# Kernel optimization log

Measured on AMD Instinct MI355X. Metric: run time of the kernel, lower is better.

Reference implementation:

```python
import jax, jax.numpy as jnp
import numpy as np

B, T, C = 8, 4096, 256
N_LAYER, LAYER_ID = 12, 5


def setup_inputs() -> dict:
    key = jax.random.key(0)
    ks = jax.random.split(key, 5)
    x = jax.random.normal(ks[0], (B, T, C), dtype=jnp.float32)
    scale = 1.0 / np.sqrt(C)
    Wk = jax.random.normal(ks[1], (C, C), jnp.float32) * scale
    Wv = jax.random.normal(ks[2], (C, C), jnp.float32) * scale
    Wr = jax.random.normal(ks[3], (C, C), jnp.float32) * scale
    Wo = jax.random.normal(ks[4], (C, C), jnp.float32) * scale
    # 'fancy' init from _init_weights
    ratio_0_to_1 = LAYER_ID / (N_LAYER - 1)
    h = np.arange(C, dtype=np.float64)
    decay = -5.0 + 8.0 * (h / (C - 1)) ** (0.7 + 1.3 * ratio_0_to_1)
    zigzag = ((np.arange(C) + 1) % 3 - 1) * 0.5
    first = np.log(0.3) + zigzag
    return dict(
        x=x, Wk=Wk, Wv=Wv, Wr=Wr, Wo=Wo,
        spatial_decay=jnp.asarray(decay, jnp.float32),
        spatial_first=jnp.asarray(first, jnp.float32),
        ln_w=jnp.ones((C,), jnp.float32),
        ln_b=jnp.zeros((C,), jnp.float32),
    )


def _wkv(w, u, k, v):
    # Numerically-stable RWKV WKV scan, matching wkv_cuda forward.
    # w, u: [C] (already divided by T); k, v: [B, T, C]. Returns y: [B, T, C].
    MIN_VALUE = -1e38

    def step(carry, kv):
        p, q, o = carry            # [B, C] each
        kt, vt = kv                # [B, C]
        no = jnp.maximum(o, u + kt)
        a = jnp.exp(o - no)
        b = jnp.exp(u + kt - no)
        y = (a * p + b * vt) / (a * q + b)
        no2 = jnp.maximum(w + o, kt)
        a2 = jnp.exp(w + o - no2)
        b2 = jnp.exp(kt - no2)
        return (a2 * p + b2 * vt, a2 * q + b2, no2), y

    p0 = jnp.zeros(k.shape[0:1] + k.shape[2:3], k.dtype)  # [B, C]
    q0 = jnp.zeros_like(p0)
    o0 = jnp.full_like(p0, MIN_VALUE)
    kT = jnp.swapaxes(k, 0, 1)  # [T, B, C]
    vT = jnp.swapaxes(v, 0, 1)
    _, yT = jax.lax.scan(step, (p0, q0, o0), (kT, vT))
    return jnp.swapaxes(yT, 0, 1)


def _layernorm(x, w, b, eps=1e-5):
    mu = jnp.mean(x, axis=-1, keepdims=True)
    xc = x - mu
    var = jnp.mean(xc * xc, axis=-1, keepdims=True)
    return xc * jax.lax.rsqrt(var + eps) * w + b


def reference(x, Wk, Wv, Wr, Wo, spatial_decay, spatial_first, ln_w, ln_b):
    # shift_pixel == 0 -> xk = xv = xr = x (module's own code path)
    t = x.shape[1]
    k = jnp.einsum('btc,dc->btd', x, Wk)
    v = jnp.einsum('btc,dc->btd', x, Wv)
    r = jnp.einsum('btc,dc->btd', x, Wr)
    sr = jax.nn.sigmoid(r)
    y = _wkv(spatial_decay / t, spatial_first / t, k, v)
    y = _layernorm(y, ln_w, ln_b)
    return jnp.einsum('btc,dc->btd', sr * y, Wo)
```

## Files before the change

kernel.cpp:

```cpp
#include <hip/hip_runtime.h>
#include <cstdint>
#include <cstddef>

#define B_ 8
#define T_ 4096
#define C_ 256
#define NC_ 256
#define L_ (T_ / NC_)
#define M_ (B_ * T_)

typedef float f32x4 __attribute__((ext_vector_type(4)));
typedef short bf16x8 __attribute__((ext_vector_type(8)));

__device__ __forceinline__ unsigned short f2b(float f) {
    unsigned int u = __float_as_uint(f);
    u += 0x7fffu + ((u >> 16) & 1u);
    return (unsigned short)(u >> 16);
}
__device__ __forceinline__ float b2f(unsigned short h) {
    return __uint_as_float(((unsigned int)h) << 16);
}

__global__ __launch_bounds__(256) void cvt_w(const float* __restrict__ Wk,
                                             const float* __restrict__ Wv,
                                             const float* __restrict__ Wr,
                                             const float* __restrict__ Wo,
                                             unsigned short* __restrict__ wb) {
    const int r = blockIdx.x;
    const int mat = r >> 5;
    const float* src = (mat == 0) ? Wk : (mat == 1) ? Wv : (mat == 2) ? Wr : Wo;
    unsigned short* dst = wb + (size_t)mat * 65536;
    const size_t i = (size_t)(r & 31) * 2048 + (size_t)threadIdx.x * 8;
    float4 a = *(const float4*)(src + i);
    float4 b = *(const float4*)(src + i + 4);
    bf16x8 o;
    o[0] = (short)f2b(a.x); o[1] = (short)f2b(a.y);
    o[2] = (short)f2b(a.z); o[3] = (short)f2b(a.w);
    o[4] = (short)f2b(b.x); o[5] = (short)f2b(b.y);
    o[6] = (short)f2b(b.z); o[7] = (short)f2b(b.w);
    *(bf16x8*)(dst + i) = o;
}

__global__ __launch_bounds__(256, 3) void gemm_qkv(const float* __restrict__ x,
                                                   const unsigned short* __restrict__ w0,
                                                   const unsigned short* __restrict__ w1,
                                                   const unsigned short* __restrict__ w2,
                                                   const float* __restrict__ decay,
                                                   unsigned short* __restrict__ kb,
                                                   unsigned short* __restrict__ vb,
                                                   unsigned short* __restrict__ b2,
                                                   float* __restrict__ sp,
                                                   float* __restrict__ sq,
                                                   float* __restrict__ so) {
    __shared__ unsigned short wlds[64 * 264];
    __shared__ float stage[4][16 * 68];
    const int tid = threadIdx.x;
    const int wave = tid >> 6, lane = tid & 63;
    const int quad = lane >> 4, l16 = lane & 15;
    const int m0 = blockIdx.x * 64 + wave * 16;
    float* myst = stage[wave];

    bf16x8 af[8];
    {
        const float* Ar = x + (size_t)(m0 + l16) * C_ + quad * 8;
#pragma unroll
        for (int kc = 0; kc < 8; ++kc) {
            float4 a = *(const float4*)(Ar + kc * 32);
            float4 b = *(const float4*)(Ar + kc * 32 + 4);
            bf16x8 o;
            o[0] = (short)f2b(a.x); o[1] = (short)f2b(a.y);
            o[2] = (short)f2b(a.z); o[3] = (short)f2b(a.w);
            o[4] = (short)f2b(b.x); o[5] = (short)f2b(b.y);
            o[6] = (short)f2b(b.z); o[7] = (short)f2b(b.w);
            af[kc] = o;
        }
    }

    const int r = tid >> 5;
    const int cs = (tid & 31) * 8;

    bf16x8 tmp[8];
#pragma unroll
    for (int it = 0; it < 8; ++it)
        tmp[it] = *(const bf16x8*)(w0 + (size_t)(it * 8 + r) * C_ + cs);

    float kreg[16], vreg[16];

    for (int s = 0; s < 4; ++s) {
        const int n0 = s * 64;
        for (int mat = 0; mat < 3; ++mat) {
            __syncthreads();
#pragma unroll
            for (int it = 0; it < 8; ++it)
                *(bf16x8*)(wlds + (it * 8 + r) * 264 + cs) = tmp[it];
            __syncthreads();

            if (!(s == 3 && mat == 2)) {
                const unsigned short* Wn = (mat == 0) ? w1 : (mat == 1) ? w2 : w0;
                const int nn = (mat == 2) ? n0 + 64 : n0;
#pragma unroll
                for (int it = 0; it < 8; ++it)
                    tmp[it] = *(const bf16x8*)(Wn + (size_t)(nn + it * 8 + r) * C_ + cs);
            }

            f32x4 acc[4];
#pragma unroll
            for (int nt = 0; nt < 4; ++nt) acc[nt] = (f32x4){0.f, 0.f, 0.f, 0.f};
#pragma unroll
            for (int nt = 0; nt < 4; ++nt) {
                const unsigned short* wrow = wlds + (nt * 16 + l16) * 264 + quad * 8;
#pragma unroll
                for (int kc = 0; kc < 8; ++kc) {
                    bf16x8 wf = *(const bf16x8*)(wrow + kc * 32);
                    acc[nt] = __builtin_amdgcn_mfma_f32_16x16x32_bf16(af[kc], wf, acc[nt], 0, 0, 0);
                }
            }

#pragma unroll
            for (int nt = 0; nt < 4; ++nt)
#pragma unroll
                for (int i = 0; i < 4; ++i)
                    myst[(quad * 4 + i) * 68 + nt * 16 + l16] = acc[nt][i];
#pragma unroll
            for (int rr = 0; rr < 4; ++rr) {
                const int row = rr * 4 + quad;
                float4 t4 = *(const float4*)&myst[row * 68 + l16 * 4];
                const size_t gidx = (size_t)(m0 + row) * C_ + n0 + l16 * 4;
                ushort4 s4;
                if (mat == 2) {
                    s4.x = f2b(1.f / (1.f + __expf(-t4.x)));
                    s4.y = f2b(1.f / (1.f + __expf(-t4.y)));
                    s4.z = f2b(1.f / (1.f + __expf(-t4.z)));
                    s4.w = f2b(1.f / (1.f + __expf(-t4.w)));
                    *(ushort4*)(b2 + gidx) = s4;
                } else {
                    s4.x = f2b(t4.x); s4.y = f2b(t4.y);
                    s4.z = f2b(t4.z); s4.w = f2b(t4.w);
                    unsigned short* Fb = (mat == 0) ? kb : vb;
                    *(ushort4*)(Fb + gidx) = s4;
                }
            }

            if (mat == 0) {
#pragma unroll
                for (int j = 0; j < L_; ++j) kreg[j] = b2f(f2b(myst[j * 68 + lane]));
            } else if (mat == 1) {
#pragma unroll
                for (int j = 0; j < L_; ++j) vreg[j] = b2f(f2b(myst[j * 68 + lane]));
                const int ch = n0 + lane;
                const float w = decay[ch] * (1.0f / T_);
                float p = 0.f, q = 0.f, o = -1e38f;
#pragma unroll
                for (int j = 0; j < L_; ++j) {
                    float wo = w + o;
                    float no = fmaxf(wo, kreg[j]);
                    float a2 = __expf(wo - no), b2s = __expf(kreg[j] - no);
                    p = a2 * p + b2s * vreg[j];
                    q = a2 * q + b2s;
                    o = no;
                }
                const int bb = m0 / T_;
                const int chunk = (m0 % T_) / L_;
                const size_t idx = ((size_t)bb * NC_ + chunk) * C_ + ch;
                sp[idx] = p; sq[idx] = q; so[idx] = o;
            }
        }
    }
}

__global__ __launch_bounds__(256, 3) void gemm_out(const unsigned short* __restrict__ A,
                                                   const unsigned short* __restrict__ w0,
                                                   float* __restrict__ f0) {
    __shared__ unsigned short wlds[64 * 264];
    __shared__ float stage[4][16 * 68];
    const int tid = threadIdx.x;
    const int wave = tid >> 6, lane = tid & 63;
    const int quad = lane >> 4, l16 = lane & 15;
    const int m0 = blockIdx.x * 64 + wave * 16;
    float* myst = stage[wave];

    bf16x8 af[8];
    {
        const unsigned short* Ar = A + (size_t)(m0 + l16) * C_ + quad * 8;
#pragma unroll
        for (int kc = 0; kc < 8; ++kc) af[kc] = *(const bf16x8*)(Ar + kc * 32);
    }

    const int r = tid >> 5;
    const int cs = (tid & 31) * 8;

    bf16x8 tmp[8];
#pragma unroll
    for (int it = 0; it < 8; ++it)
        tmp[it] = *(const bf16x8*)(w0 + (size_t)(it * 8 + r) * C_ + cs);

    for (int s = 0; s < 4; ++s) {
        const int n0 = s * 64;
        __syncthreads();
#pragma unroll
        for (int it = 0; it < 8; ++it)
            *(bf16x8*)(wlds + (it * 8 + r) * 264 + cs) = tmp[it];
        __syncthreads();

        if (s < 3) {
#pragma unroll
            for (int it = 0; it < 8; ++it)
                tmp[it] = *(const bf16x8*)(w0 + (size_t)(n0 + 64 + it * 8 + r) * C_ + cs);
        }

        f32x4 acc[4];
#pragma unroll
        for (int nt = 0; nt < 4; ++nt) acc[nt] = (f32x4){0.f, 0.f, 0.f, 0.f};
#pragma unroll
        for (int nt = 0; nt < 4; ++nt) {
            const unsigned short* wrow = wlds + (nt * 16 + l16) * 264 + quad * 8;
#pragma unroll
            for (int kc = 0; kc < 8; ++kc) {
                bf16x8 wf = *(const bf16x8*)(wrow + kc * 32);
                acc[nt] = __builtin_amdgcn_mfma_f32_16x16x32_bf16(af[kc], wf, acc[nt], 0, 0, 0);
            }
        }

#pragma unroll
        for (int nt = 0; nt < 4; ++nt)
#pragma unroll
            for (int i = 0; i < 4; ++i)
                myst[(quad * 4 + i) * 68 + nt * 16 + l16] = acc[nt][i];
#pragma unroll
        for (int rr = 0; rr < 4; ++rr) {
            const int row = rr * 4 + quad;
            float4 t4 = *(const float4*)&myst[row * 68 + l16 * 4];
            *(float4*)(f0 + (size_t)(m0 + row) * C_ + n0 + l16 * 4) = t4;
        }
    }
}

__global__ __launch_bounds__(256) void wkv_combine_par(const float* __restrict__ decay,
                                                       float* __restrict__ sp,
                                                       float* __restrict__ sq,
                                                       float* __restrict__ so) {
    __shared__ float tp[16][17], tq[16][17], to[16][17];
    const int tid = threadIdx.x;
    const int cgi = tid >> 4;
    const int cl = tid & 15;
    const int b = blockIdx.x;
    const int c = blockIdx.y * 16 + cl;
    const float wL = decay[c] * (1.0f / T_) * (float)L_;
    const float wL16 = wL * 16.0f;
    const size_t base = ((size_t)b * NC_ + (size_t)cgi * 16) * C_ + c;

    float p = 0.f, q = 0.f, o = -1e38f;
#pragma unroll 4
    for (int j = 0; j < 16; ++j) {
        size_t idx = base + (size_t)j * C_;
        float lp = sp[idx], lq = sq[idx], lo = so[idx];
        float ow = o + wL;
        float no = fmaxf(ow, lo);
        float ea = __expf(ow - no), eb = __expf(lo - no);
        p = ea * p + eb * lp;
        q = ea * q + eb * lq;
        o = no;
    }
    tp[cgi][cl] = p; tq[cgi][cl] = q; to[cgi][cl] = o;

    float ip = p, iq = q, io = o;
#pragma unroll
    for (int off = 1; off < 16; off <<= 1) {
        __syncthreads();
        float ap = 0.f, aq = 0.f, ao = 0.f;
        const bool doit = (cgi >= off);
        if (doit) { ap = tp[cgi - off][cl]; aq = tq[cgi - off][cl]; ao = to[cgi - off][cl]; }
        __syncthreads();
        if (doit) {
            float ow = ao + (float)off * wL16;
            float no = fmaxf(ow, io);
            float ea = __expf(ow - no), eb = __expf(io - no);
            ip = ea * ap + eb * ip;
            iq = ea * aq + eb * iq;
            io = no;
            tp[cgi][cl] = ip; tq[cgi][cl] = iq; to[cgi][cl] = io;
        }
    }
    __syncthreads();

    float ep, eq, eo;
    if (cgi == 0) { ep = 0.f; eq = 0.f; eo = -1e38f; }
    else          { ep = tp[cgi - 1][cl]; eq = tq[cgi - 1][cl]; eo = to[cgi - 1][cl]; }

    for (int j = 0; j < 16; ++j) {
        size_t idx = base + (size_t)j * C_;
        float lp = sp[idx], lq = sq[idx], lo = so[idx];
        sp[idx] = ep; sq[idx] = eq; so[idx] = eo;
        float ow = eo + wL;
        float no = fmaxf(ow, lo);
        float ea = __expf(ow - no), eb = __expf(lo - no);
        ep = ea * ep + eb * lp;
        eq = ea * eq + eb * lq;
        eo = no;
    }
}

__global__ __launch_bounds__(256, 8) void wkv_pass2_ln(const unsigned short* __restrict__ k,
                                                       const unsigned short* __restrict__ v,
                                                       const unsigned short* __restrict__ sr,
                                                       const float* __restrict__ decay,
                                                       const float* __restrict__ first,
                                                       const float* __restrict__ lw,
                                                       const float* __restrict__ lb,
                                                       const float* __restrict__ sp,
                                                       const float* __restrict__ sq,
                                                       const float* __restrict__ so,
                                                       unsigned short* __restrict__ z) {
    __shared__ float tile[16][264];
    __shared__ float mu_s[16], rs_s[16];
    const int c = threadIdx.x, chunk = blockIdx.x, b = blockIdx.y;
    const int wave = c >> 6, lane = c & 63;
    const float w = decay[c] * (1.0f / T_);
    const float u = first[c] * (1.0f / T_);
    const float gw = lw[c], gb = lb[c];
    size_t sidx = ((size_t)b * NC_ + chunk) * C_ + c;
    float p = sp[sidx], q = sq[sidx], o = so[sidx];
    size_t base = ((size_t)b * T_ + (size_t)chunk * L_) * C_ + c;

    for (int t = 0; t < L_; t += 8) {
        float kk[8], vv[8];
#pragma unroll
        for (int j = 0; j < 8; ++j) {
            kk[j] = b2f(k[base + (size_t)(t + j) * C_]);
            vv[j] = b2f(v[base + (size_t)(t + j) * C_]);
        }
#pragma unroll
        for (int j = 0; j < 8; ++j) {
            float uk = u + kk[j];
            float no = fmaxf(o, uk);
            float a = __expf(o - no), bb = __expf(uk - no);
            tile[t + j][c] = (a * p + bb * vv[j]) / (a * q + bb);
            float wo = w + o;
            float no2 = fmaxf(wo, kk[j]);
            float a2 = __expf(wo - no2), b2 = __expf(kk[j] - no2);
            p = a2 * p + b2 * vv[j];
            q = a2 * q + b2;
            o = no2;
        }
    }
    __syncthreads();
#pragma unroll
    for (int r = 0; r < 4; ++r) {
        const int j = wave * 4 + r;
        float4 t4 = *(const float4*)&tile[j][lane * 4];
        float s = t4.x + t4.y + t4.z + t4.w;
        float ss = t4.x * t4.x + t4.y * t4.y + t4.z * t4.z + t4.w * t4.w;
#pragma unroll
        for (int m = 1; m < 64; m <<= 1) {
            s += __shfl_xor(s, m, 64);
            ss += __shfl_xor(ss, m, 64);
        }
        if (lane == 0) {
            float mu = s * (1.f / C_);
            mu_s[j] = mu;
            rs_s[j] = rsqrtf(ss * (1.f / C_) - mu * mu + 1e-5f);
        }
    }
    __syncthreads();
#pragma unroll
    for (int j = 0; j < L_; ++j) {
        float zz = (tile[j][c] - mu_s[j]) * rs_s[j] * gw + gb;
        zz *= b2f(sr[base + (size_t)j * C_]);
        z[base + (size_t)j * C_] = f2b(zz);
    }
}

extern "C" void kernel_launch(void* const* d_in, const int* in_sizes, int n_in,
                              void* d_out, int out_size, void* d_ws, size_t ws_size,
                              hipStream_t stream) {
    const float* x     = (const float*)d_in[0];
    const float* Wk    = (const float*)d_in[1];
    const float* Wv    = (const float*)d_in[2];
    const float* Wr    = (const float*)d_in[3];
    const float* Wo    = (const float*)d_in[4];
    const float* decay = (const float*)d_in[5];
    const float* first = (const float*)d_in[6];
    const float* lnw   = (const float*)d_in[7];
    const float* lnb   = (const float*)d_in[8];
    float* out = (float*)d_out;

    char* ws = (char*)d_ws;
    const size_t NE = (size_t)M_ * C_;
    unsigned short* wb  = (unsigned short*)ws; ws += 4 * 65536 * 2;
    unsigned short* kbuf = (unsigned short*)ws; ws += NE * 2;
    unsigned short* vbuf = (unsigned short*)ws; ws += NE * 2;
    unsigned short* srb = (unsigned short*)ws; ws += NE * 2;
    unsigned short* zb  = (unsigned short*)ws; ws += NE * 2;
    const size_t SE = (size_t)B_ * NC_ * C_;
    float* sp = (float*)ws; ws += SE * 4;
    float* sq = (float*)ws; ws += SE * 4;
    float* so = (float*)ws; ws += SE * 4;
    unsigned short* wkb = wb;
    unsigned short* wvb = wb + 65536;
    unsigned short* wrb = wb + 2 * 65536;
    unsigned short* wob = wb + 3 * 65536;

    cvt_w<<<128, 256, 0, stream>>>(Wk, Wv, Wr, Wo, wb);

    gemm_qkv<<<dim3(M_ / 64), 256, 0, stream>>>(x, wkb, wvb, wrb, decay,
                                                kbuf, vbuf, srb, sp, sq, so);

    wkv_combine_par<<<dim3(B_, C_ / 16), 256, 0, stream>>>(decay, sp, sq, so);
    wkv_pass2_ln<<<dim3(NC_, B_), 256, 0, stream>>>(kbuf, vbuf, srb, decay, first,
                                                    lnw, lnb, sp, sq, so, zb);

    gemm_out<<<dim3(M_ / 64), 256, 0, stream>>>(zb, wob, out);
}
```

Before: 157.3 us.

## Store k, v, sigmoid(r) in chunk-major channel layout for vectorized scan loads

The projection GEMM now writes k, v and sigmoid(r) in a layout where each channel's 16 time steps within a chunk are contiguous, using two 16-byte stores per lane instead of strided ushort4 row stores. The chunked WKV/layernorm kernel then reads each channel's k, v and sr as two bf16x8 vector loads instead of 16 strided scalar loads. This aims to cut memory transactions on both the write and read side of the intermediates. Stores from a wave now hit 64 separate 32-byte segments, which may coalesce less well than the earlier row-contiguous writes.

```diff
diff --git a/kernel.cpp b/kernel.cpp
--- a/kernel.cpp
+++ b/kernel.cpp
@@ -78,6 +78,9 @@
 
     const int r = tid >> 5;
     const int cs = (tid & 31) * 8;
+    const int bb = m0 / T_;
+    const int chunk = (m0 % T_) / L_;
+    const size_t colbase = ((size_t)bb * NC_ + chunk) * C_;
 
     bf16x8 tmp[8];
 #pragma unroll
@@ -121,33 +124,36 @@
 #pragma unroll
                 for (int i = 0; i < 4; ++i)
                     myst[(quad * 4 + i) * 68 + nt * 16 + l16] = acc[nt][i];
-#pragma unroll
-            for (int rr = 0; rr < 4; ++rr) {
-                const int row = rr * 4 + quad;
-                float4 t4 = *(const float4*)&myst[row * 68 + l16 * 4];
-                const size_t gidx = (size_t)(m0 + row) * C_ + n0 + l16 * 4;
-                ushort4 s4;
-                if (mat == 2) {
-                    s4.x = f2b(1.f / (1.f + __expf(-t4.x)));
-                    s4.y = f2b(1.f / (1.f + __expf(-t4.y)));
-                    s4.z = f2b(1.f / (1.f + __expf(-t4.z)));
-                    s4.w = f2b(1.f / (1.f + __expf(-t4.w)));
-                    *(ushort4*)(b2 + gidx) = s4;
-                } else {
-                    s4.x = f2b(t4.x); s4.y = f2b(t4.y);
-                    s4.z = f2b(t4.z); s4.w = f2b(t4.w);
-                    unsigned short* Fb = (mat == 0) ? kb : vb;
-                    *(ushort4*)(Fb + gidx) = s4;
+
+            const int ch = n0 + lane;
+            unsigned short* dst = (mat == 0) ? kb : (mat == 1) ? vb : b2;
+            unsigned short* cd = dst + (colbase + ch) * 16;
+            if (mat == 0) {
+                bf16x8 p0, p1;
+#pragma unroll
+                for (int j = 0; j < 8; ++j) p0[j] = (short)f2b(myst[j * 68 + lane]);
+#pragma unroll
+                for (int j = 0; j < 8; ++j) p1[j] = (short)f2b(myst[(8 + j) * 68 + lane]);
+                *(bf16x8*)(cd) = p0;
+                *(bf16x8*)(cd + 8) = p1;
+#pragma unroll
+                for (int j = 0; j < 8; ++j) {
+                    kreg[j] = b2f((unsigned short)p0[j]);
+                    kreg[8 + j] = b2f((unsigned short)p1[j]);
                 }
-            }
-
-            if (mat == 0) {
-#pragma unroll
-                for (int j = 0; j < L_; ++j) kreg[j] = b2f(f2b(myst[j * 68 + lane]));
             } else if (mat == 1) {
-#pragma unroll
-                for (int j = 0; j < L_; ++j) vreg[j] = b2f(f2b(myst[j * 68 + lane]));
-                const int ch = n0 + lane;
+                bf16x8 p0, p1;
+#pragma unroll
+                for (int j = 0; j < 8; ++j) p0[j] = (short)f2b(myst[j * 68 + lane]);
+#pragma unroll
+                for (int j = 0; j < 8; ++j) p1[j] = (short)f2b(myst[(8 + j) * 68 + lane]);
+                *(bf16x8*)(cd) = p0;
+                *(bf16x8*)(cd + 8) = p1;
+#pragma unroll
+                for (int j = 0; j < 8; ++j) {
+                    vreg[j] = b2f((unsigned short)p0[j]);
+                    vreg[8 + j] = b2f((unsigned short)p1[j]);
+                }
                 const float w = decay[ch] * (1.0f / T_);
                 float p = 0.f, q = 0.f, o = -1e38f;
 #pragma unroll
@@ -159,10 +165,18 @@
                     q = a2 * q + b2s;
                     o = no;
                 }
-                const int bb = m0 / T_;
-                const int chunk = (m0 % T_) / L_;
-                const size_t idx = ((size_t)bb * NC_ + chunk) * C_ + ch;
+                const size_t idx = colbase + ch;
                 sp[idx] = p; sq[idx] = q; so[idx] = o;
+            } else {
+                bf16x8 p0, p1;
+#pragma unroll
+                for (int j = 0; j < 8; ++j)
+                    p0[j] = (short)f2b(1.f / (1.f + __expf(-myst[j * 68 + lane])));
+#pragma unroll
+                for (int j = 0; j < 8; ++j)
+                    p1[j] = (short)f2b(1.f / (1.f + __expf(-myst[(8 + j) * 68 + lane])));
+                *(bf16x8*)(cd) = p0;
+                *(bf16x8*)(cd + 8) = p1;
             }
         }
     }
@@ -322,26 +336,25 @@
     float p = sp[sidx], q = sq[sidx], o = so[sidx];
     size_t base = ((size_t)b * T_ + (size_t)chunk * L_) * C_ + c;
 
-    for (int t = 0; t < L_; t += 8) {
-        float kk[8], vv[8];
-#pragma unroll
-        for (int j = 0; j < 8; ++j) {
-            kk[j] = b2f(k[base + (size_t)(t + j) * C_]);
-            vv[j] = b2f(v[base + (size_t)(t + j) * C_]);
-        }
-#pragma unroll
-        for (int j = 0; j < 8; ++j) {
-            float uk = u + kk[j];
-            float no = fmaxf(o, uk);
-            float a = __expf(o - no), bb = __expf(uk - no);
-            tile[t + j][c] = (a * p + bb * vv[j]) / (a * q + bb);
-            float wo = w + o;
-            float no2 = fmaxf(wo, kk[j]);
-            float a2 = __expf(wo - no2), b2 = __expf(kk[j] - no2);
-            p = a2 * p + b2 * vv[j];
-            q = a2 * q + b2;
-            o = no2;
-        }
+    const unsigned short* kp = k + sidx * 16;
+    const unsigned short* vp = v + sidx * 16;
+    bf16x8 k0 = *(const bf16x8*)(kp), k1 = *(const bf16x8*)(kp + 8);
+    bf16x8 v0 = *(const bf16x8*)(vp), v1 = *(const bf16x8*)(vp + 8);
+
+#pragma unroll
+    for (int j = 0; j < L_; ++j) {
+        float kj = b2f((unsigned short)((j < 8) ? k0[j] : k1[j - 8]));
+        float vj = b2f((unsigned short)((j < 8) ? v0[j] : v1[j - 8]));
+        float uk = u + kj;
+        float no = fmaxf(o, uk);
+        float a = __expf(o - no), bb = __expf(uk - no);
+        tile[j][c] = (a * p + bb * vj) / (a * q + bb);
+        float wo = w + o;
+        float no2 = fmaxf(wo, kj);
+        float a2 = __expf(wo - no2), b2 = __expf(kj - no2);
+        p = a2 * p + b2 * vj;
+        q = a2 * q + b2;
+        o = no2;
     }
     __syncthreads();
 #pragma unroll
@@ -362,10 +375,12 @@
         }
     }
     __syncthreads();
+    const unsigned short* srp = sr + sidx * 16;
+    bf16x8 s0 = *(const bf16x8*)(srp), s1 = *(const bf16x8*)(srp + 8);
 #pragma unroll
     for (int j = 0; j < L_; ++j) {
         float zz = (tile[j][c] - mu_s[j]) * rs_s[j] * gw + gb;
-        zz *= b2f(sr[base + (size_t)j * C_]);
+        zz *= b2f((unsigned short)((j < 8) ? s0[j] : s1[j - 8]));
         z[base + (size_t)j * C_] = f2b(zz);
     }
 }
```

New measurement: 159.2 us. Within noise of the previous version (+1.2%).

## Double-buffer weight tiles in LDS and stage bf16 outputs in gemm_qkv

Applied to the files above, without the earlier changes.

Splits the shared weight tile into two buffers so the next weight tile is written to the idle buffer after compute. This cuts the two barriers per tile to one. The output staging buffer now holds bf16 values, with conversion and sigmoid applied before the LDS write, which halves staging traffic and removes the redundant round-trip conversion. Shared memory use rises by about 34 KB per block, which may lower occupancy below the requested three blocks per CU.

```diff
diff --git a/kernel.cpp b/kernel.cpp
--- a/kernel.cpp
+++ b/kernel.cpp
@@ -52,13 +52,13 @@
                                                    float* __restrict__ sp,
                                                    float* __restrict__ sq,
                                                    float* __restrict__ so) {
-    __shared__ unsigned short wlds[64 * 264];
-    __shared__ float stage[4][16 * 68];
+    __shared__ unsigned short wlds[2][64 * 264];
+    __shared__ unsigned short stg[4][16 * 72];
     const int tid = threadIdx.x;
     const int wave = tid >> 6, lane = tid & 63;
     const int quad = lane >> 4, l16 = lane & 15;
     const int m0 = blockIdx.x * 64 + wave * 16;
-    float* myst = stage[wave];
+    unsigned short* myst = stg[wave];
 
     bf16x8 af[8];
     {
@@ -83,19 +83,20 @@
 #pragma unroll
     for (int it = 0; it < 8; ++it)
         tmp[it] = *(const bf16x8*)(w0 + (size_t)(it * 8 + r) * C_ + cs);
+    unsigned short* wrd = wlds[0];
+    unsigned short* wwr = wlds[1];
+#pragma unroll
+    for (int it = 0; it < 8; ++it)
+        *(bf16x8*)(wrd + (it * 8 + r) * 264 + cs) = tmp[it];
+    __syncthreads();
 
     float kreg[16], vreg[16];
 
     for (int s = 0; s < 4; ++s) {
         const int n0 = s * 64;
         for (int mat = 0; mat < 3; ++mat) {
-            __syncthreads();
-#pragma unroll
-            for (int it = 0; it < 8; ++it)
-                *(bf16x8*)(wlds + (it * 8 + r) * 264 + cs) = tmp[it];
-            __syncthreads();
-
-            if (!(s == 3 && mat == 2)) {
+            const bool last = (s == 3 && mat == 2);
+            if (!last) {
                 const unsigned short* Wn = (mat == 0) ? w1 : (mat == 1) ? w2 : w0;
                 const int nn = (mat == 2) ? n0 + 64 : n0;
 #pragma unroll
@@ -108,7 +109,7 @@
             for (int nt = 0; nt < 4; ++nt) acc[nt] = (f32x4){0.f, 0.f, 0.f, 0.f};
 #pragma unroll
             for (int nt = 0; nt < 4; ++nt) {
-                const unsigned short* wrow = wlds + (nt * 16 + l16) * 264 + quad * 8;
+                const unsigned short* wrow = wrd + (nt * 16 + l16) * 264 + quad * 8;
 #pragma unroll
                 for (int kc = 0; kc < 8; ++kc) {
                     bf16x8 wf = *(const bf16x8*)(wrow + kc * 32);
@@ -116,37 +117,34 @@
                 }
             }
 
-#pragma unroll
-            for (int nt = 0; nt < 4; ++nt)
-#pragma unroll
-                for (int i = 0; i < 4; ++i)
-                    myst[(quad * 4 + i) * 68 + nt * 16 + l16] = acc[nt][i];
+            if (mat == 2) {
+#pragma unroll
+                for (int nt = 0; nt < 4; ++nt)
+#pragma unroll
+                    for (int i = 0; i < 4; ++i)
+                        myst[(quad * 4 + i) * 72 + nt * 16 + l16] =
+                            f2b(1.f / (1.f + __expf(-acc[nt][i])));
+            } else {
+#pragma unroll
+                for (int nt = 0; nt < 4; ++nt)
+#pragma unroll
+                    for (int i = 0; i < 4; ++i)
+                        myst[(quad * 4 + i) * 72 + nt * 16 + l16] = f2b(acc[nt][i]);
+            }
+            unsigned short* dstb = (mat == 0) ? kb : (mat == 1) ? vb : b2;
 #pragma unroll
             for (int rr = 0; rr < 4; ++rr) {
                 const int row = rr * 4 + quad;
-                float4 t4 = *(const float4*)&myst[row * 68 + l16 * 4];
-                const size_t gidx = (size_t)(m0 + row) * C_ + n0 + l16 * 4;
-                ushort4 s4;
-                if (mat == 2) {
-                    s4.x = f2b(1.f / (1.f + __expf(-t4.x)));
-                    s4.y = f2b(1.f / (1.f + __expf(-t4.y)));
-                    s4.z = f2b(1.f / (1.f + __expf(-t4.z)));
-                    s4.w = f2b(1.f / (1.f + __expf(-t4.w)));
-                    *(ushort4*)(b2 + gidx) = s4;
-                } else {
-                    s4.x = f2b(t4.x); s4.y = f2b(t4.y);
-                    s4.z = f2b(t4.z); s4.w = f2b(t4.w);
-                    unsigned short* Fb = (mat == 0) ? kb : vb;
-                    *(ushort4*)(Fb + gidx) = s4;
-                }
+                ushort4 t4 = *(const ushort4*)&myst[row * 72 + l16 * 4];
+                *(ushort4*)(dstb + (size_t)(m0 + row) * C_ + n0 + l16 * 4) = t4;
             }
 
             if (mat == 0) {
 #pragma unroll
-                for (int j = 0; j < L_; ++j) kreg[j] = b2f(f2b(myst[j * 68 + lane]));
+                for (int j = 0; j < L_; ++j) kreg[j] = b2f(myst[j * 72 + lane]);
             } else if (mat == 1) {
 #pragma unroll
-                for (int j = 0; j < L_; ++j) vreg[j] = b2f(f2b(myst[j * 68 + lane]));
+                for (int j = 0; j < L_; ++j) vreg[j] = b2f(myst[j * 72 + lane]);
                 const int ch = n0 + lane;
                 const float w = decay[ch] * (1.0f / T_);
                 float p = 0.f, q = 0.f, o = -1e38f;
@@ -163,6 +161,14 @@
                 const int chunk = (m0 % T_) / L_;
                 const size_t idx = ((size_t)bb * NC_ + chunk) * C_ + ch;
                 sp[idx] = p; sq[idx] = q; so[idx] = o;
+            }
+
+            if (!last) {
+#pragma unroll
+                for (int it = 0; it < 8; ++it)
+                    *(bf16x8*)(wwr + (it * 8 + r) * 264 + cs) = tmp[it];
+                unsigned short* t = wrd; wrd = wwr; wwr = t;
+                __syncthreads();
             }
         }
     }
```

Measured after the change: 157.0 us. About the same (-0.2%).
